# Kernel tuning notes

Measured on AMD Instinct MI355X. Metric: run time of the kernel, lower is better.

The kernel has to match this reference:

```python
import jax, jax.numpy as jnp
import numpy as np

CODEBOOK_SIZE = 8192
TEMP = 1.0  # sample_codebook_temp


def l2norm(t, eps=1e-12):
    # matches F.normalize(t, p=2, dim=-1)
    n = jnp.sqrt(jnp.sum(t * t, axis=-1, keepdims=True))
    return t / jnp.maximum(n, eps)


def setup_inputs() -> dict:
    key = jax.random.key(0)
    kx, ke = jax.random.split(key)
    x = jax.random.normal(kx, (1, 16, 1024, 512), dtype=jnp.float32)
    # learned codebook, stored l2-normalized as in uniform_init -> l2norm
    embed = l2norm(jax.random.normal(ke, (1, 8192, 512), dtype=jnp.float32))
    return {"x": x, "embed": embed}


def reference(x, embed):
    # x: [h, b, n, d]  embed: [h, c, d]
    h, d = x.shape[0], x.shape[-1]
    shape = x.shape
    flatten = l2norm(x.reshape(h, -1, d))          # transform_input = l2norm, pack 'h * d'
    embed_n = l2norm(embed)                        # cosine-sim codebook
    # cosine similarity logits: [h, N, c]
    dist = jnp.einsum('hnd,hcd->hnc', flatten, embed_n)
    # gumbel_sample with stochastic=False: plain argmax of logits
    embed_ind = jnp.argmax(dist, axis=-1)          # [h, N]
    one_hot = jax.nn.one_hot(embed_ind, CODEBOOK_SIZE, dtype=dist.dtype)
    # straight-through (learnable codebook, training): hard + soft - sg(soft)
    soft = jax.nn.softmax(dist / TEMP, axis=-1)
    one_hot_st = one_hot + soft - jax.lax.stop_gradient(soft)
    # quantize via one-hot mix of codebook vectors: [h, N, d]
    quantize = jnp.einsum('hnc,hcd->hnd', one_hot_st, embed_n)
    quantize = quantize.reshape(shape)
    embed_ind = embed_ind.reshape(shape[:-1])
    return quantize, embed_ind, dist
```

## Files before the change

kernel.cpp:

```cpp
#include <hip/hip_runtime.h>
#include <math.h>

#define N_ROWS 16384
#define C_CODES 8192
#define DIM 512
#define I_OFS (N_ROWS * DIM)
#define D_OFS (I_OFS + N_ROWS)

typedef __bf16 bf16;
typedef bf16 bf16x8 __attribute__((ext_vector_type(8)));
typedef float f32x4 __attribute__((ext_vector_type(4)));

__device__ __forceinline__ void gload16(void* lds, const void* g) {
  __builtin_amdgcn_global_load_lds((__attribute__((address_space(1))) void*)(g),
                                   (__attribute__((address_space(3))) void*)(lds), 16, 0, 0);
}

__global__ void norm_embed(const float* __restrict__ embed, float* __restrict__ en,
                           bf16* __restrict__ enb) {
  int wave = threadIdx.x >> 6, lane = threadIdx.x & 63;
  int row = blockIdx.x * 4 + wave;
  const float* src = embed + (size_t)row * DIM;
  float4 v0 = ((const float4*)src)[lane * 2];
  float4 v1 = ((const float4*)src)[lane * 2 + 1];
  float s = v0.x * v0.x + v0.y * v0.y + v0.z * v0.z + v0.w * v0.w +
            v1.x * v1.x + v1.y * v1.y + v1.z * v1.z + v1.w * v1.w;
  for (int m = 1; m < 64; m <<= 1) s += __shfl_xor(s, m, 64);
  float nrm = fmaxf(sqrtf(s), 1e-12f);
  float4 o0, o1;
  o0.x = v0.x / nrm; o0.y = v0.y / nrm; o0.z = v0.z / nrm; o0.w = v0.w / nrm;
  o1.x = v1.x / nrm; o1.y = v1.y / nrm; o1.z = v1.z / nrm; o1.w = v1.w / nrm;
  float* dst = en + (size_t)row * DIM;
  ((float4*)dst)[lane * 2] = o0;
  ((float4*)dst)[lane * 2 + 1] = o1;
  bf16x8 b;
  b[0] = (bf16)o0.x; b[1] = (bf16)o0.y; b[2] = (bf16)o0.z; b[3] = (bf16)o0.w;
  b[4] = (bf16)o1.x; b[5] = (bf16)o1.y; b[6] = (bf16)o1.z; b[7] = (bf16)o1.w;
  *(bf16x8*)(enb + (size_t)row * DIM + lane * 8) = b;
}

__global__ void norm_x(const float* __restrict__ x, bf16* __restrict__ xnb,
                       float* __restrict__ xnorm) {
  int wave = threadIdx.x >> 6, lane = threadIdx.x & 63;
  int row = blockIdx.x * 4 + wave;
  const float* src = x + (size_t)row * DIM;
  float4 v0 = ((const float4*)src)[lane * 2];
  float4 v1 = ((const float4*)src)[lane * 2 + 1];
  float s = v0.x * v0.x + v0.y * v0.y + v0.z * v0.z + v0.w * v0.w +
            v1.x * v1.x + v1.y * v1.y + v1.z * v1.z + v1.w * v1.w;
  for (int m = 1; m < 64; m <<= 1) s += __shfl_xor(s, m, 64);
  float nrm = fmaxf(sqrtf(s), 1e-12f);
  if (lane == 0) xnorm[row] = nrm;
  bf16x8 b;
  b[0] = (bf16)(v0.x / nrm); b[1] = (bf16)(v0.y / nrm);
  b[2] = (bf16)(v0.z / nrm); b[3] = (bf16)(v0.w / nrm);
  b[4] = (bf16)(v1.x / nrm); b[5] = (bf16)(v1.y / nrm);
  b[6] = (bf16)(v1.z / nrm); b[7] = (bf16)(v1.w / nrm);
  *(bf16x8*)(xnb + (size_t)row * DIM + lane * 8) = b;
}

#define BM 128
#define BN 128
#define BK 32

__global__ __launch_bounds__(256, 2) void gemm_dist(
    const bf16* __restrict__ xnb, const bf16* __restrict__ enb,
    float* __restrict__ dist, float* __restrict__ tilemax) {
  __shared__ bf16 As[BM * BK];
  __shared__ bf16 Bs[BN * BK];
  __shared__ float wmax[2][128];

  int tid = threadIdx.x;
  int cb = blockIdx.x;
  int rb = blockIdx.y;
  int rowBase = rb * BM, colBase = cb * BN;
  int wave = tid >> 6, lane = tid & 63;
  int wr = wave >> 1, wc = wave & 1;
  int row16 = lane & 15, quad = lane >> 4;

  f32x4 acc[4][4];
  f32x4 zero = {0.f, 0.f, 0.f, 0.f};
  for (int i = 0; i < 4; ++i)
    for (int j = 0; j < 4; ++j) acc[i][j] = zero;

  int e0 = tid * 8;
  int e1 = 2048 + tid * 8;
  int m0 = e0 >> 5, k0 = e0 & 31;
  int m1 = e1 >> 5, k1 = e1 & 31;
  const bf16* ga0 = xnb + (size_t)(rowBase + m0) * DIM + k0;
  const bf16* ga1 = xnb + (size_t)(rowBase + m1) * DIM + k1;
  const bf16* gb0 = enb + (size_t)(colBase + m0) * DIM + k0;
  const bf16* gb1 = enb + (size_t)(colBase + m1) * DIM + k1;

  for (int kt = 0; kt < DIM / BK; ++kt) {
    int ko = kt * BK;
    gload16(&As[e0], ga0 + ko);
    gload16(&As[e1], ga1 + ko);
    gload16(&Bs[e0], gb0 + ko);
    gload16(&Bs[e1], gb1 + ko);
    __syncthreads();
    bf16x8 a[4], b[4];
    for (int i = 0; i < 4; ++i)
      a[i] = *(const bf16x8*)&As[(wr * 64 + i * 16 + row16) * BK + quad * 8];
    for (int j = 0; j < 4; ++j)
      b[j] = *(const bf16x8*)&Bs[(wc * 64 + j * 16 + row16) * BK + quad * 8];
    for (int i = 0; i < 4; ++i)
      for (int j = 0; j < 4; ++j)
        acc[i][j] = __builtin_amdgcn_mfma_f32_16x16x32_bf16(a[i], b[j], acc[i][j], 0, 0, 0);
    __syncthreads();
  }

  for (int i = 0; i < 4; ++i) {
    int gr = rowBase + wr * 64 + i * 16 + quad * 4;
    for (int j = 0; j < 4; ++j) {
      int gc = colBase + wc * 64 + j * 16 + row16;
      for (int r = 0; r < 4; ++r)
        dist[(size_t)(gr + r) * C_CODES + gc] = acc[i][j][r];
    }
  }

  for (int i = 0; i < 4; ++i) {
    float rm[4];
    for (int r = 0; r < 4; ++r)
      rm[r] = fmaxf(fmaxf(acc[i][0][r], acc[i][1][r]), fmaxf(acc[i][2][r], acc[i][3][r]));
    for (int m = 1; m < 16; m <<= 1)
      for (int r = 0; r < 4; ++r) rm[r] = fmaxf(rm[r], __shfl_xor(rm[r], m, 64));
    if (row16 == 0)
      for (int r = 0; r < 4; ++r) wmax[wc][wr * 64 + i * 16 + quad * 4 + r] = rm[r];
  }
  __syncthreads();
  if (tid < 128) {
    float m = fmaxf(wmax[0][tid], wmax[1][tid]);
    tilemax[(size_t)(rowBase + tid) * 64 + cb] = m;
  }
}

#define EPS 0.01f

__global__ __launch_bounds__(256) void refine(
    const float* __restrict__ x, const float* __restrict__ en,
    const float* __restrict__ xnorm, const float* __restrict__ tilemax,
    const float* __restrict__ dist, float* __restrict__ out) {
  int wave = threadIdx.x >> 6, lane = threadIdx.x & 63;
  int r = blockIdx.x * 4 + wave;

  float tmv = tilemax[(size_t)r * 64 + lane];
  float m = tmv;
#pragma unroll
  for (int s = 1; s < 64; s <<= 1) m = fmaxf(m, __shfl_xor(m, s, 64));
  float T = m - EPS;

  const float* xr = x + (size_t)r * DIM;
  float4 xv0 = ((const float4*)xr)[lane * 2];
  float4 xv1 = ((const float4*)xr)[lane * 2 + 1];
  float nrm = xnorm[r];

  const float* drow = dist + (size_t)r * C_CODES;
  float bv = -3.0e38f;
  int bi = 0x7fffffff;

  unsigned long long smask = __ballot(tmv >= T);
  while (smask) {
    int cbB = __builtin_ctzll(smask);
    smask &= smask - 1;
    int base = cbB * 128;
    float v0 = drow[base + lane];
    float v1 = drow[base + 64 + lane];
    unsigned long long b0 = __ballot(v0 >= T);
    unsigned long long b1 = __ballot(v1 >= T);
    while (b0 | b1) {
      int c;
      if (b0) {
        int l = __builtin_ctzll(b0); b0 &= b0 - 1; c = base + l;
      } else {
        int l = __builtin_ctzll(b1); b1 &= b1 - 1; c = base + 64 + l;
      }
      const float* er = en + (size_t)c * DIM;
      float4 e0 = ((const float4*)er)[lane * 2];
      float4 e1 = ((const float4*)er)[lane * 2 + 1];
      float d = xv0.x * e0.x + xv0.y * e0.y + xv0.z * e0.z + xv0.w * e0.w +
                xv1.x * e1.x + xv1.y * e1.y + xv1.z * e1.z + xv1.w * e1.w;
#pragma unroll
      for (int s = 1; s < 64; s <<= 1) d += __shfl_xor(d, s, 64);
      float v = d / nrm;
      if (v > bv || (v == bv && c < bi)) { bv = v; bi = c; }
    }
  }

  if (lane == 0) out[I_OFS + r] = (float)bi;
  const float* eb = en + (size_t)bi * DIM;
  float4 q0 = ((const float4*)eb)[lane * 2];
  float4 q1 = ((const float4*)eb)[lane * 2 + 1];
  float* orow = out + (size_t)r * DIM;
  ((float4*)orow)[lane * 2] = q0;
  ((float4*)orow)[lane * 2 + 1] = q1;
}

extern "C" void kernel_launch(void* const* d_in, const int* in_sizes, int n_in,
                              void* d_out, int out_size, void* d_ws, size_t ws_size,
                              hipStream_t stream) {
  const float* x = (const float*)d_in[0];
  const float* embed = (const float*)d_in[1];
  float* out = (float*)d_out;
  char* ws = (char*)d_ws;
  bf16* enb = (bf16*)(ws);
  bf16* xnb = (bf16*)(ws + 8388608);
  float* en = (float*)(ws + 25165824);
  float* xnorm = (float*)(ws + 41943040);
  float* tilemax = (float*)(ws + 42008576);

  hipLaunchKernelGGL(norm_embed, dim3(C_CODES / 4), dim3(256), 0, stream, embed, en, enb);
  hipLaunchKernelGGL(norm_x, dim3(N_ROWS / 4), dim3(256), 0, stream, x, xnb, xnorm);
  hipLaunchKernelGGL(gemm_dist, dim3(C_CODES / BN, N_ROWS / BM), dim3(256), 0, stream,
                     xnb, enb, out + D_OFS, tilemax);
  hipLaunchKernelGGL(refine, dim3(N_ROWS / 4), dim3(256), 0, stream,
                     x, en, xnorm, tilemax, out + D_OFS, out);
}
```

Baseline: 739.9 us.

## Rewrite distance GEMM as 256x256 tile with double-buffered swizzled LDS pipeline

Result: slower. 763.3 us (+3.2%).

```diff
diff --git a/kernel.cpp b/kernel.cpp
--- a/kernel.cpp
+++ b/kernel.cpp
@@ -59,79 +59,146 @@
   *(bf16x8*)(xnb + (size_t)row * DIM + lane * 8) = b;
 }
 
-#define BM 128
-#define BN 128
-#define BK 32
-
-__global__ __launch_bounds__(256, 2) void gemm_dist(
+
+#define SB __builtin_amdgcn_sched_barrier(0)
+#define BARR __builtin_amdgcn_s_barrier()
+#define WLG do { asm volatile("s_waitcnt lgkmcnt(0)" ::: "memory"); SB; } while (0)
+
+__device__ __forceinline__ void stage_hh(char* sm, const bf16* pA, const bf16* pB,
+                                         int tid, int j) {
+  if (j >= 32) return;
+  int tau = j >> 2, hh = j & 3, d = tau & 1;
+  const bf16* p = (hh >= 2) ? pA : pB;
+  int half = hh & 1;
+  int opb = (hh >= 2) ? 0 : 32768;
+  size_t go = (size_t)(half * 128) * DIM + (size_t)tau * 64;
+  char* db = sm + d * 65536 + opb + half * 16384 + tid * 16;
+  gload16(db, p + go);
+  gload16(db + 8192, p + go + (size_t)64 * DIM);
+}
+
+__global__ __launch_bounds__(512, 1) void gemm_dist(
     const bf16* __restrict__ xnb, const bf16* __restrict__ enb,
     float* __restrict__ dist, float* __restrict__ tilemax) {
-  __shared__ bf16 As[BM * BK];
-  __shared__ bf16 Bs[BN * BK];
-  __shared__ float wmax[2][128];
+  __shared__ char sm[131072];
 
   int tid = threadIdx.x;
-  int cb = blockIdx.x;
-  int rb = blockIdx.y;
-  int rowBase = rb * BM, colBase = cb * BN;
+  int bid = blockIdx.x;
+  int swz = (bid & 7) * 256 + (bid >> 3);
+  int rb = swz >> 5, cb = swz & 31;
+  int rowBase = rb * 256, colBase = cb * 256;
   int wave = tid >> 6, lane = tid & 63;
-  int wr = wave >> 1, wc = wave & 1;
+  int wr = wave >> 2, wc = wave & 3;
   int row16 = lane & 15, quad = lane >> 4;
 
-  f32x4 acc[4][4];
+  int trow = tid >> 3;
+  int kel = ((tid & 7) ^ (trow & 7)) << 3;
+  const bf16* pA = xnb + (size_t)(rowBase + trow) * DIM + kel;
+  const bf16* pB = enb + (size_t)(colBase + trow) * DIM + kel;
+
+  int msk = (row16 & 7) << 4;
+  int o0 = row16 * 128 + ((quad << 4) ^ msk);
+  int o1 = row16 * 128 + (((quad << 4) | 64) ^ msk);
+
+  f32x4 acc[8][4];
   f32x4 zero = {0.f, 0.f, 0.f, 0.f};
-  for (int i = 0; i < 4; ++i)
+#pragma unroll
+  for (int i = 0; i < 8; ++i)
+#pragma unroll
     for (int j = 0; j < 4; ++j) acc[i][j] = zero;
 
-  int e0 = tid * 8;
-  int e1 = 2048 + tid * 8;
-  int m0 = e0 >> 5, k0 = e0 & 31;
-  int m1 = e1 >> 5, k1 = e1 & 31;
-  const bf16* ga0 = xnb + (size_t)(rowBase + m0) * DIM + k0;
-  const bf16* ga1 = xnb + (size_t)(rowBase + m1) * DIM + k1;
-  const bf16* gb0 = enb + (size_t)(colBase + m0) * DIM + k0;
-  const bf16* gb1 = enb + (size_t)(colBase + m1) * DIM + k1;
-
-  for (int kt = 0; kt < DIM / BK; ++kt) {
-    int ko = kt * BK;
-    gload16(&As[e0], ga0 + ko);
-    gload16(&As[e1], ga1 + ko);
-    gload16(&Bs[e0], gb0 + ko);
-    gload16(&Bs[e1], gb1 + ko);
-    __syncthreads();
-    bf16x8 a[4], b[4];
-    for (int i = 0; i < 4; ++i)
-      a[i] = *(const bf16x8*)&As[(wr * 64 + i * 16 + row16) * BK + quad * 8];
-    for (int j = 0; j < 4; ++j)
-      b[j] = *(const bf16x8*)&Bs[(wc * 64 + j * 16 + row16) * BK + quad * 8];
-    for (int i = 0; i < 4; ++i)
-      for (int j = 0; j < 4; ++j)
-        acc[i][j] = __builtin_amdgcn_mfma_f32_16x16x32_bf16(a[i], b[j], acc[i][j], 0, 0, 0);
-    __syncthreads();
-  }
+  bf16x8 a[4][2], b01[2][2], b23[2][2];
+
+#define LDA(mh) do { _Pragma("unroll") for (int m = 0; m < 4; ++m) { \
+      a[m][0] = *(const bf16x8*)(aB + (mh) * 8192 + m * 2048 + o0); \
+      a[m][1] = *(const bf16x8*)(aB + (mh) * 8192 + m * 2048 + o1); } } while (0)
+#define LDB(breg, pr) do { _Pragma("unroll") for (int n = 0; n < 2; ++n) { \
+      breg[n][0] = *(const bf16x8*)(bB + ((pr) * 2 + n) * 2048 + o0); \
+      breg[n][1] = *(const bf16x8*)(bB + ((pr) * 2 + n) * 2048 + o1); } } while (0)
+#define MF(mh, pr, breg) do { _Pragma("unroll") for (int m = 0; m < 4; ++m) \
+      _Pragma("unroll") for (int n = 0; n < 2; ++n) { \
+        acc[(mh)*4+m][(pr)*2+n] = __builtin_amdgcn_mfma_f32_16x16x32_bf16( \
+            a[m][0], breg[n][0], acc[(mh)*4+m][(pr)*2+n], 0, 0, 0); \
+        acc[(mh)*4+m][(pr)*2+n] = __builtin_amdgcn_mfma_f32_16x16x32_bf16( \
+            a[m][1], breg[n][1], acc[(mh)*4+m][(pr)*2+n], 0, 0, 0); \
+      } } while (0)
+
+  for (int j = 0; j < 7; ++j) stage_hh(sm, pA, pB, tid, j);
+  asm volatile("s_waitcnt vmcnt(6)" ::: "memory"); SB;
+  BARR; SB;
+
+#define TILE(t, d) do { \
+    const char* aB = sm + (d) * 65536 + wr * 16384; \
+    const char* bB = sm + (d) * 65536 + 32768 + (wc >> 1) * 16384 + (wc & 1) * 8192; \
+     \
+    LDA(0); LDB(b23, 1); \
+    stage_hh(sm, pA, pB, tid, 4 * (t) + 7); \
+    SB; BARR; WLG; \
+    __builtin_amdgcn_s_setprio(1); MF(0, 1, b23); __builtin_amdgcn_s_setprio(0); \
+    SB; BARR; SB; \
+     \
+    LDB(b01, 0); \
+    SB; BARR; WLG; \
+    __builtin_amdgcn_s_setprio(1); MF(0, 0, b01); __builtin_amdgcn_s_setprio(0); \
+    SB; BARR; SB; \
+     \
+    LDA(1); \
+    stage_hh(sm, pA, pB, tid, 4 * (t) + 8); \
+    SB; BARR; WLG; \
+    __builtin_amdgcn_s_setprio(1); MF(1, 0, b01); __builtin_amdgcn_s_setprio(0); \
+    SB; BARR; SB; \
+     \
+    stage_hh(sm, pA, pB, tid, 4 * (t) + 9); \
+    stage_hh(sm, pA, pB, tid, 4 * (t) + 10); \
+    SB; BARR; SB; \
+    __builtin_amdgcn_s_setprio(1); MF(1, 1, b23); __builtin_amdgcn_s_setprio(0); \
+    SB; \
+    if ((t) < 6) { asm volatile("s_waitcnt vmcnt(6)" ::: "memory"); } \
+    else         { asm volatile("s_waitcnt vmcnt(0)" ::: "memory"); } \
+    SB; BARR; SB; \
+  } while (0)
 
   for (int i = 0; i < 4; ++i) {
-    int gr = rowBase + wr * 64 + i * 16 + quad * 4;
-    for (int j = 0; j < 4; ++j) {
-      int gc = colBase + wc * 64 + j * 16 + row16;
-      for (int r = 0; r < 4; ++r)
-        dist[(size_t)(gr + r) * C_CODES + gc] = acc[i][j][r];
+    int t0 = 2 * i;
+    TILE(t0, 0);
+    TILE(t0 + 1, 1);
+  }
+
+  float (*wmax)[256] = (float(*)[256])sm;
+#pragma unroll
+  for (int m = 0; m < 8; ++m) {
+    float rm[4];
+#pragma unroll
+    for (int r = 0; r < 4; ++r)
+      rm[r] = fmaxf(fmaxf(acc[m][0][r], acc[m][1][r]), fmaxf(acc[m][2][r], acc[m][3][r]));
+#pragma unroll
+    for (int s = 1; s < 16; s <<= 1)
+#pragma unroll
+      for (int r = 0; r < 4; ++r) rm[r] = fmaxf(rm[r], __shfl_xor(rm[r], s, 64));
+    if (row16 == 0)
+#pragma unroll
+      for (int r = 0; r < 4; ++r) wmax[wc][wr * 128 + m * 16 + quad * 4 + r] = rm[r];
+  }
+
+#pragma unroll
+  for (int m = 0; m < 8; ++m) {
+#pragma unroll
+    for (int r = 0; r < 4; ++r) {
+      size_t grow = (size_t)(rowBase + wr * 128 + m * 16 + quad * 4 + r);
+      float* dp = dist + grow * C_CODES + colBase + wc * 64 + row16;
+#pragma unroll
+      for (int n = 0; n < 4; ++n) dp[n * 16] = acc[m][n][r];
     }
   }
 
-  for (int i = 0; i < 4; ++i) {
-    float rm[4];
-    for (int r = 0; r < 4; ++r)
-      rm[r] = fmaxf(fmaxf(acc[i][0][r], acc[i][1][r]), fmaxf(acc[i][2][r], acc[i][3][r]));
-    for (int m = 1; m < 16; m <<= 1)
-      for (int r = 0; r < 4; ++r) rm[r] = fmaxf(rm[r], __shfl_xor(rm[r], m, 64));
-    if (row16 == 0)
-      for (int r = 0; r < 4; ++r) wmax[wc][wr * 64 + i * 16 + quad * 4 + r] = rm[r];
-  }
   __syncthreads();
-  if (tid < 128) {
-    float m = fmaxf(wmax[0][tid], wmax[1][tid]);
-    tilemax[(size_t)(rowBase + tid) * 64 + cb] = m;
+  if (tid < 256) {
+    float v = fmaxf(wmax[0][tid], wmax[1][tid]);
+    tilemax[(size_t)(rowBase + tid) * 64 + cb * 2] = v;
+  } else {
+    int rr = tid - 256;
+    float v = fmaxf(wmax[2][rr], wmax[3][rr]);
+    tilemax[(size_t)(rowBase + rr) * 64 + cb * 2 + 1] = v;
   }
 }
 
@@ -211,7 +278,7 @@
 
   hipLaunchKernelGGL(norm_embed, dim3(C_CODES / 4), dim3(256), 0, stream, embed, en, enb);
   hipLaunchKernelGGL(norm_x, dim3(N_ROWS / 4), dim3(256), 0, stream, x, xnb, xnorm);
-  hipLaunchKernelGGL(gemm_dist, dim3(C_CODES / BN, N_ROWS / BM), dim3(256), 0, stream,
+  hipLaunchKernelGGL(gemm_dist, dim3(2048), dim3(512), 0, stream,
                      xnb, enb, out + D_OFS, tilemax);
   hipLaunchKernelGGL(refine, dim3(N_ROWS / 4), dim3(256), 0, stream,
                      x, en, xnorm, tilemax, out + D_OFS, out);
```
